# Performance work log

Measured on AMD Instinct MI355X. Metric: run time of the kernel, lower is better.

Reference implementation:

```python
import jax, jax.numpy as jnp
import numpy as np

N_NODES = 100000
N_EDGES = 1600000
NUM_GRAPHS = 1000
NODE_IN, EDGE_IN = 32, 16
NODE_EMB, EDGE_EMB, HID, OUT, L = 64, 32, 64, 1, 3
EPS = 1e-5


def _glorot(key, shape):
    fan_in = shape[0]
    return jax.random.normal(key, shape, jnp.float32) / np.sqrt(fan_in)


def setup_inputs() -> dict:
    key = jax.random.key(0)
    ks = jax.random.split(key, 16)
    inp = {
        "x": jax.random.normal(ks[0], (N_NODES, NODE_IN), jnp.float32),
        "edge_attr": jax.random.normal(ks[1], (N_EDGES, EDGE_IN), jnp.float32),
        "edge_index": jax.random.randint(ks[2], (2, N_EDGES), 0, N_NODES, jnp.int64
                                         if jax.config.jax_enable_x64 else jnp.int32),
        "batch": jnp.sort(jax.random.randint(ks[3], (N_NODES,), 0, NUM_GRAPHS)),
        # embeddings
        "node_W": _glorot(ks[4], (NODE_IN, NODE_EMB)),
        "node_b": jnp.zeros((NODE_EMB,), jnp.float32),
        "edge_W": _glorot(ks[5], (EDGE_IN, EDGE_EMB)),
        "edge_b": jnp.zeros((EDGE_EMB,), jnp.float32),
        # per-layer MPNN params (node_dim==64 for every layer since node_emb_dim==hidden_dim)
        "msg_W": _glorot(ks[6], (L, NODE_EMB + EDGE_EMB, HID)),
        "msg_b": jnp.zeros((L, HID), jnp.float32),
        "msg_gamma": jnp.ones((L, HID), jnp.float32),
        "msg_beta": jnp.zeros((L, HID), jnp.float32),
        "upd_W": _glorot(ks[7], (L, NODE_EMB + HID, HID)),
        "upd_b": jnp.zeros((L, HID), jnp.float32),
        "upd_gamma": jnp.ones((L, HID), jnp.float32),
        "upd_beta": jnp.zeros((L, HID), jnp.float32),
        # readout
        "r1_W": _glorot(ks[8], (HID, HID)),
        "r1_b": jnp.zeros((HID,), jnp.float32),
        "r2_W": _glorot(ks[9], (HID, OUT)),
        "r2_b": jnp.zeros((OUT,), jnp.float32),
    }
    return inp


def _bn(h, gamma, beta):
    # BatchNorm1d in training mode: normalize with batch mean / biased variance
    mu = jnp.mean(h, axis=0)
    var = jnp.mean(jnp.square(h - mu), axis=0)
    return gamma * (h - mu) * jax.lax.rsqrt(var + EPS) + beta


def reference(x, edge_attr, edge_index, batch,
              node_W, node_b, edge_W, edge_b,
              msg_W, msg_b, msg_gamma, msg_beta,
              upd_W, upd_b, upd_gamma, upd_beta,
              r1_W, r1_b, r2_W, r2_b):
    h = x @ node_W + node_b                       # [N, 64]
    e = edge_attr @ edge_W + edge_b               # [E, 32]
    src, dst = edge_index[0], edge_index[1]
    for i in range(L):
        # message: gather x_j, concat edge feats, Linear-ReLU-BN (dropout = eval/no-op)
        m = jnp.concatenate([h[src], e], axis=-1) @ msg_W[i] + msg_b[i]   # [E, 64]
        m = _bn(jax.nn.relu(m), msg_gamma[i], msg_beta[i])
        # aggregate: scatter-add to destination nodes
        agg = jax.ops.segment_sum(m, dst, num_segments=N_NODES)          # [N, 64]
        # update: concat self feats, Linear-ReLU-BN
        u = jnp.concatenate([h, agg], axis=-1) @ upd_W[i] + upd_b[i]     # [N, 64]
        h = _bn(jax.nn.relu(u), upd_gamma[i], upd_beta[i])
    # global add pool over graphs
    g = jax.ops.segment_sum(h, batch, num_segments=NUM_GRAPHS)           # [G, 64]
    out = jax.nn.relu(g @ r1_W + r1_b) @ r2_W + r2_b                     # [G, 1]
    return out
```

## Files before the change

### kernel.cpp

```cpp
#include <hip/hip_runtime.h>
#include <hip/hip_bf16.h>

#define N_NODES   100000
#define N_EDGES   1600000
#define NUM_GRAPHS 1000

typedef unsigned int u32;
typedef unsigned short u16;

typedef __bf16 bf16_t;
typedef bf16_t bf16x8 __attribute__((ext_vector_type(8)));
typedef float  f32x4  __attribute__((ext_vector_type(4)));

__device__ __forceinline__ float bf2f(u16 u){ return __uint_as_float(((u32)u)<<16); }
__device__ __forceinline__ float BL(u32 u){ return __uint_as_float(u<<16); }
__device__ __forceinline__ float BH(u32 u){ return __uint_as_float(u&0xffff0000u); }
__device__ __forceinline__ u16 f2bf(float f){
  u32 u = __float_as_uint(f);
  return (u16)((u + 0x7fffu + ((u>>16)&1u)) >> 16);
}
__device__ __forceinline__ float ldf(const void* p, size_t i, int isbf){
  return isbf ? bf2f(((const u16*)p)[i]) : ((const float*)p)[i];
}

__global__ void k_detect(const u32* __restrict__ x, int* __restrict__ flag){
  int t = threadIdx.x; int cnt = 0;
  for (int i = t; i < 256; i += 64){
    u32 w = x[i];
    u32 e = (w >> 7) & 0xffu;
    if (e >= 110u && e <= 137u) cnt++;
  }
  for (int o = 32; o; o >>= 1) cnt += __shfl_xor(cnt, o);
  if (t == 0) *flag = (cnt > 128) ? 1 : 0;
}

__global__ void k_prep(const void* __restrict__ eW, const void* __restrict__ eb,
                       const void* __restrict__ mW, const void* __restrict__ mb,
                       u16* __restrict__ Wcol, const int* __restrict__ flagp){
  int isbf = *flagp;
  int l = blockIdx.x, c = threadIdx.x;
  u16* W = Wcol + ((size_t)l*64 + c)*96;
  for (int k = 0; k < 64; k++)
    W[k] = f2bf(ldf(mW, (size_t)(l*96 + k)*64 + c, isbf));
  for (int j = 0; j < 16; j++){
    float acc = 0.f;
    for (int k = 0; k < 32; k++)
      acc += ldf(eW, (size_t)j*32 + k, isbf) * ldf(mW, (size_t)(l*96 + 64 + k)*64 + c, isbf);
    W[64 + j] = f2bf(acc);
  }
  float fbv = ldf(mb, (size_t)l*64 + c, isbf);
  for (int k = 0; k < 32; k++)
    fbv += ldf(eb, k, isbf) * ldf(mW, (size_t)(l*96 + 64 + k)*64 + c, isbf);
  W[80] = f2bf(fbv);
  for (int k = 81; k < 96; k++) W[k] = 0;
}

__global__ void k_node_emb(const void* __restrict__ x, const void* __restrict__ nW,
                           const void* __restrict__ nb, float* __restrict__ h,
                           u16* __restrict__ h_bf, const int* __restrict__ flagp){
  int isbf = *flagp;
  int lane = threadIdx.x & 63;
  int gw = (blockIdx.x*blockDim.x + threadIdx.x) >> 6;
  int nw = (gridDim.x*blockDim.x) >> 6;
  float w[32];
#pragma unroll
  for (int k = 0; k < 32; k++) w[k] = ldf(nW, (size_t)k*64 + lane, isbf);
  float bias = ldf(nb, lane, isbf);
  for (int n = gw; n < N_NODES; n += nw){
    float acc = bias;
    if (isbf){
      const uint4* xr = (const uint4*)((const u16*)x + (size_t)n*32);
#pragma unroll
      for (int q = 0; q < 4; q++){
        uint4 a = xr[q];
        u32 uu[4] = {a.x, a.y, a.z, a.w};
#pragma unroll
        for (int j = 0; j < 4; j++){
          acc = fmaf(BL(uu[j]), w[q*8 + 2*j + 0], acc);
          acc = fmaf(BH(uu[j]), w[q*8 + 2*j + 1], acc);
        }
      }
    } else {
      const float4* xr = (const float4*)((const float*)x + (size_t)n*32);
#pragma unroll
      for (int q = 0; q < 8; q++){
        float4 a = xr[q];
        acc = fmaf(a.x, w[q*4+0], acc); acc = fmaf(a.y, w[q*4+1], acc);
        acc = fmaf(a.z, w[q*4+2], acc); acc = fmaf(a.w, w[q*4+3], acc);
      }
    }
    h[(size_t)n*64 + lane] = acc;
    h_bf[(size_t)n*64 + lane] = f2bf(acc);
  }
}

__global__ void k_deg(const int* __restrict__ ei, int* __restrict__ deg){
  int i = blockIdx.x*blockDim.x + threadIdx.x;
  int stride = gridDim.x*blockDim.x;
  for (int e = i; e < N_EDGES; e += stride)
    atomicAdd(&deg[ei[N_EDGES + e]], 1);
}

__global__ void __launch_bounds__(256) k_scan1(const int* __restrict__ deg,
                                               int* __restrict__ bsum){
  __shared__ int wsum[4];
  int b = blockIdx.x, t = threadIdx.x;
  int i0 = b*512 + t;
  int s = 0;
  if (i0 < N_NODES) s += deg[i0];
  if (i0 + 256 < N_NODES) s += deg[i0 + 256];
  for (int o = 32; o; o >>= 1) s += __shfl_xor(s, o);
  if ((t & 63) == 0) wsum[t >> 6] = s;
  __syncthreads();
  if (t == 0) bsum[b] = wsum[0] + wsum[1] + wsum[2] + wsum[3];
}

__global__ void k_scan2(const int* __restrict__ bsum, int* __restrict__ boff,
                        int* __restrict__ rp){
  __shared__ int l[200];
  int t = threadIdx.x;
  if (t < 196) l[t] = bsum[t];
  __syncthreads();
  if (t == 0){
    int r = 0;
    for (int k = 0; k < 196; k++){ int x = l[k]; l[k] = r; r += x; }
    rp[N_NODES] = r;
  }
  __syncthreads();
  if (t < 196) boff[t] = l[t];
}

__global__ void __launch_bounds__(256) k_scan3(const int* __restrict__ deg,
                        const int* __restrict__ boff, int* __restrict__ rp,
                        int* __restrict__ cursor, float* __restrict__ degf){
  __shared__ int wpre[4];
  int b = blockIdx.x, t = threadIdx.x;
  int i0 = b*512 + 2*t;
  int d0 = (i0     < N_NODES) ? deg[i0]     : 0;
  int d1 = (i0 + 1 < N_NODES) ? deg[i0 + 1] : 0;
  int s = d0 + d1;
  int incl = s;
  for (int o = 1; o < 64; o <<= 1){ int u = __shfl_up(incl, o); if ((t & 63) >= o) incl += u; }
  if ((t & 63) == 63) wpre[t >> 6] = incl;
  __syncthreads();
  if (t == 0){ int r = 0; for (int k = 0; k < 4; k++){ int x = wpre[k]; wpre[k] = r; r += x; } }
  __syncthreads();
  int excl = boff[b] + wpre[t >> 6] + incl - s;
  if (i0 < N_NODES){
    rp[i0] = excl; cursor[i0] = excl; degf[i0] = (float)d0;
  }
  if (i0 + 1 < N_NODES){
    rp[i0+1] = excl + d0; cursor[i0+1] = excl + d0; degf[i0+1] = (float)d1;
  }
}

__global__ void k_scatter(const int* __restrict__ ei, int* __restrict__ cursor,
                          int* __restrict__ perm2){
  int i = blockIdx.x*blockDim.x + threadIdx.x;
  int stride = gridDim.x*blockDim.x;
  for (int e = i; e < N_EDGES; e += stride){
    int d = ei[N_EDGES + e];
    int p = atomicAdd(&cursor[d], 1);
    ((int2*)perm2)[p] = make_int2(ei[e], e);
  }
}

__global__ void __launch_bounds__(256) k_msgmm(
    const u16* __restrict__ h_bf, const void* __restrict__ ea,
    const int* __restrict__ rp, const int* __restrict__ perm2,
    const u16* __restrict__ Wcol, float* __restrict__ agg,
    float* __restrict__ stats, const int* __restrict__ flagp,
    int l, int nwaves){
  __shared__ float bs[128];
  __shared__ u32 lds[4*16*52];
  int tid = threadIdx.x;
  if (tid < 128) bs[tid] = 0.f;
  int lane = tid & 63, wv = tid >> 6;
  u32* A = lds + wv*16*52;
  int isbf = *flagp;
  if (lane < 32){
    uint4 z = make_uint4((lane&1)? 0u : 0x3f80u, 0u, 0u, 0u);
    *(uint4*)(A + (lane>>1)*52 + 40 + (lane&1)*4) = z;
  }
  __syncthreads();
  int w = blockIdx.x*4 + wv;
  long long t0 = (long long)w     * N_EDGES / nwaves;
  long long t1 = (long long)(w+1) * N_EDGES / nwaves;
  int lo = 0, hi = N_NODES;
  while (lo < hi){ int mid = (lo+hi)>>1; if ((long long)rp[mid] < t0) lo = mid+1; else hi = mid; }
  int n0 = lo, n1;
  if (w == nwaves-1) n1 = N_NODES;
  else {
    lo = 0; hi = N_NODES;
    while (lo < hi){ int mid = (lo+hi)>>1; if ((long long)rp[mid] < t1) lo = mid+1; else hi = mid; }
    n1 = lo;
  }
  int nn = lane & 15, kg = lane >> 4;
  bf16x8 B[3][4];
  const u16* Wl = Wcol + (size_t)l*64*96;
#pragma unroll
  for (int t = 0; t < 4; t++)
#pragma unroll
    for (int kb = 0; kb < 3; kb++)
      B[kb][t] = *(const bf16x8*)(Wl + (size_t)(t*16+nn)*96 + kb*32 + kg*8);
  float s1[4] = {0,0,0,0}, s2[4] = {0,0,0,0};
  int rA = lane>>3, sA = lane&7;
  int rC = lane>>1, sC = lane&1;
  for (int n = n0; n < n1; n++){
    int b0 = rp[n], b1 = rp[n+1];
    float r0 = 0.f, r1 = 0.f, r2 = 0.f, r3 = 0.f;
    for (int base = b0; base < b1; base += 16){
      int rem = b1 - base; if (rem > 16) rem = 16;
      int eA = base + (rA < rem ? rA : rem-1);
      int2 pA = ((const int2*)perm2)[eA];
      uint4 vA = ((const uint4*)h_bf)[(size_t)pA.x*8 + sA];
      int rB = rA + 8;
      int eB = base + (rB < rem ? rB : rem-1);
      int2 pB = ((const int2*)perm2)[eB];
      uint4 vB = ((const uint4*)h_bf)[(size_t)pB.x*8 + sA];
      uint4 vC; int doC = (lane < 32);
      if (doC){
        int eC = base + (rC < rem ? rC : rem-1);
        int2 pC = ((const int2*)perm2)[eC];
        if (isbf){
          vC = ((const uint4*)ea)[(size_t)pC.y*2 + sC];
        } else {
          const float4* ef = (const float4*)ea;
          float4 f0 = ef[(size_t)pC.y*4 + sC*2];
          float4 f1 = ef[(size_t)pC.y*4 + sC*2 + 1];
          vC.x = (u32)f2bf(f0.x) | ((u32)f2bf(f0.y)<<16);
          vC.y = (u32)f2bf(f0.z) | ((u32)f2bf(f0.w)<<16);
          vC.z = (u32)f2bf(f1.x) | ((u32)f2bf(f1.y)<<16);
          vC.w = (u32)f2bf(f1.z) | ((u32)f2bf(f1.w)<<16);
        }
      }
      asm volatile("s_waitcnt lgkmcnt(0)" ::: "memory");
      *(uint4*)(A + rA*52 + sA*4) = vA;
      *(uint4*)(A + rB*52 + sA*4) = vB;
      if (doC) *(uint4*)(A + rC*52 + 32 + sC*4) = vC;
      asm volatile("s_waitcnt lgkmcnt(0)" ::: "memory");
      f32x4 a0 = {0,0,0,0}, a1 = {0,0,0,0}, a2 = {0,0,0,0}, a3 = {0,0,0,0};
#pragma unroll
      for (int kb = 0; kb < 3; kb++){
        bf16x8 af = *(const bf16x8*)(A + nn*52 + kb*16 + kg*4);
        a0 = __builtin_amdgcn_mfma_f32_16x16x32_bf16(af, B[kb][0], a0, 0,0,0);
        a1 = __builtin_amdgcn_mfma_f32_16x16x32_bf16(af, B[kb][1], a1, 0,0,0);
        a2 = __builtin_amdgcn_mfma_f32_16x16x32_bf16(af, B[kb][2], a2, 0,0,0);
        a3 = __builtin_amdgcn_mfma_f32_16x16x32_bf16(af, B[kb][3], a3, 0,0,0);
      }
      int rowbase = kg*4;
      float ts0 = 0.f, ts1 = 0.f, ts2 = 0.f, ts3 = 0.f;
#pragma unroll
      for (int j = 0; j < 4; j++){
        bool valid = (rowbase + j) < rem;
        float m0 = fmaxf(a0[j], 0.f); m0 = valid ? m0 : 0.f;
        float m1 = fmaxf(a1[j], 0.f); m1 = valid ? m1 : 0.f;
        float m2 = fmaxf(a2[j], 0.f); m2 = valid ? m2 : 0.f;
        float m3 = fmaxf(a3[j], 0.f); m3 = valid ? m3 : 0.f;
        ts0 += m0; ts1 += m1; ts2 += m2; ts3 += m3;
        s2[0] = fmaf(m0,m0,s2[0]); s2[1] = fmaf(m1,m1,s2[1]);
        s2[2] = fmaf(m2,m2,s2[2]); s2[3] = fmaf(m3,m3,s2[3]);
      }
      s1[0] += ts0; s1[1] += ts1; s1[2] += ts2; s1[3] += ts3;
      ts0 += __shfl_xor(ts0,16); ts0 += __shfl_xor(ts0,32);
      ts1 += __shfl_xor(ts1,16); ts1 += __shfl_xor(ts1,32);
      ts2 += __shfl_xor(ts2,16); ts2 += __shfl_xor(ts2,32);
      ts3 += __shfl_xor(ts3,16); ts3 += __shfl_xor(ts3,32);
      r0 += ts0; r1 += ts1; r2 += ts2; r3 += ts3;
    }
    float v = (kg==0) ? r0 : (kg==1) ? r1 : (kg==2) ? r2 : r3;
    agg[(size_t)n*64 + lane] = v;
  }
#pragma unroll
  for (int t = 0; t < 4; t++){
    atomicAdd(&bs[t*16+nn], s1[t]);
    atomicAdd(&bs[64+t*16+nn], s2[t]);
  }
  __syncthreads();
  if (tid < 128) atomicAdd(&stats[tid], bs[tid]);
}

__global__ void k_fin(const float* __restrict__ stats, const void* __restrict__ gamma,
                      const void* __restrict__ beta, float* __restrict__ aff,
                      float cnt_inv, int goff, const int* __restrict__ flagp){
  int isbf = *flagp; int c = threadIdx.x;
  float mu  = stats[c]      * cnt_inv;
  float var = stats[64 + c] * cnt_inv - mu*mu;
  float rs  = rsqrtf(var + 1e-5f);
  float g = ldf(gamma, (size_t)goff + c, isbf);
  float b = ldf(beta,  (size_t)goff + c, isbf);
  aff[c]      = g*rs;
  aff[64 + c] = b - g*mu*rs;
}

__global__ void __launch_bounds__(256) k_upd(
    float* __restrict__ h, const float* __restrict__ agg,
    const float* __restrict__ degf, const float* __restrict__ maff,
    const void* __restrict__ uW, const void* __restrict__ ub,
    float* __restrict__ stats, const int* __restrict__ flagp, int l){
  __shared__ float bs[128];
  if (threadIdx.x < 128) bs[threadIdx.x] = 0.f;
  __syncthreads();
  int isbf = *flagp;
  int lane = threadIdx.x & 63;
  int gw = (blockIdx.x*blockDim.x + threadIdx.x) >> 6;
  int nw = (gridDim.x*blockDim.x) >> 6;
  float wa[64], wb[64]; float tv = 0.f;
#pragma unroll
  for (int k = 0; k < 64; k++){
    wa[k] = ldf(uW, (size_t)(l*128 + k)*64 + lane, isbf);
    float wk = ldf(uW, (size_t)(l*128 + 64 + k)*64 + lane, isbf);
    wb[k] = wk * maff[k];
    tv = fmaf(maff[64 + k], wk, tv);
  }
  float bias = ldf(ub, (size_t)l*64 + lane, isbf);
  float s1 = 0.f, s2 = 0.f;
  for (int n = gw; n < N_NODES; n += nw){
    const float4* hr = (const float4*)(h + (size_t)n*64);
    const float4* ar = (const float4*)(agg + (size_t)n*64);
    float a0 = fmaf(degf[n], tv, bias), a1 = 0.f, a2 = 0.f, a3 = 0.f;
#pragma unroll
    for (int q = 0; q < 8; q++){
      float4 a = hr[2*q+0];
      a0 = fmaf(a.x, wa[8*q+0], a0); a0 = fmaf(a.y, wa[8*q+1], a0);
      a0 = fmaf(a.z, wa[8*q+2], a0); a0 = fmaf(a.w, wa[8*q+3], a0);
      float4 b = hr[2*q+1];
      a1 = fmaf(b.x, wa[8*q+4], a1); a1 = fmaf(b.y, wa[8*q+5], a1);
      a1 = fmaf(b.z, wa[8*q+6], a1); a1 = fmaf(b.w, wa[8*q+7], a1);
      float4 c = ar[2*q+0];
      a2 = fmaf(c.x, wb[8*q+0], a2); a2 = fmaf(c.y, wb[8*q+1], a2);
      a2 = fmaf(c.z, wb[8*q+2], a2); a2 = fmaf(c.w, wb[8*q+3], a2);
      float4 d = ar[2*q+1];
      a3 = fmaf(d.x, wb[8*q+4], a3); a3 = fmaf(d.y, wb[8*q+5], a3);
      a3 = fmaf(d.z, wb[8*q+6], a3); a3 = fmaf(d.w, wb[8*q+7], a3);
    }
    float rl = fmaxf((a0 + a1) + (a2 + a3), 0.f);
    h[(size_t)n*64 + lane] = rl;
    s1 += rl;
    s2 = fmaf(rl, rl, s2);
  }
  atomicAdd(&bs[lane], s1);
  atomicAdd(&bs[64 + lane], s2);
  __syncthreads();
  if (threadIdx.x < 128) atomicAdd(&stats[threadIdx.x], bs[threadIdx.x]);
}

__global__ void k_norm(float* __restrict__ h, const float* __restrict__ uaff,
                       u16* __restrict__ h_bf){
  int i = blockIdx.x*blockDim.x + threadIdx.x;
  if (i >= N_NODES*16) return;
  int c4 = i & 15;
  float4 sq = *(const float4*)(uaff + 4*c4);
  float4 tq = *(const float4*)(uaff + 64 + 4*c4);
  float4 v = ((const float4*)h)[i];
  float4 o;
  o.x = fmaf(sq.x, v.x, tq.x); o.y = fmaf(sq.y, v.y, tq.y);
  o.z = fmaf(sq.z, v.z, tq.z); o.w = fmaf(sq.w, v.w, tq.w);
  ((float4*)h)[i] = o;
  ushort4 ob;
  ob.x = f2bf(o.x); ob.y = f2bf(o.y); ob.z = f2bf(o.z); ob.w = f2bf(o.w);
  ((ushort4*)h_bf)[i] = ob;
}

__global__ void k_pool(const float* __restrict__ h, const int* __restrict__ batch,
                       float* __restrict__ g){
  int lane = threadIdx.x & 63;
  int gw = (blockIdx.x*blockDim.x + threadIdx.x) >> 6;
  int nw = (gridDim.x*blockDim.x) >> 6;
  int chunk = (N_NODES + nw - 1) / nw;
  int n0 = gw*chunk;
  int n1 = n0 + chunk; if (n1 > N_NODES) n1 = N_NODES;
  int cur = -1; float acc = 0.f;
  for (int n = n0; n < n1; n++){
    int b = batch[n];
    float v = h[(size_t)n*64 + lane];
    if (b != cur){
      if (cur >= 0) atomicAdd(&g[(size_t)cur*64 + lane], acc);
      cur = b; acc = v;
    } else acc += v;
  }
  if (cur >= 0) atomicAdd(&g[(size_t)cur*64 + lane], acc);
}

__global__ void k_read(const float* __restrict__ g, const void* __restrict__ r1W,
                       const void* __restrict__ r1b, const void* __restrict__ r2W,
                       const void* __restrict__ r2b, void* __restrict__ out,
                       const int* __restrict__ flagp){
  int isbf = *flagp;
  int lane = threadIdx.x;
  int gr = blockIdx.x;
  float w[64];
#pragma unroll
  for (int k = 0; k < 64; k++) w[k] = ldf(r1W, (size_t)k*64 + lane, isbf);
  float acc = ldf(r1b, lane, isbf);
  const float4* grow = (const float4*)(g + (size_t)gr*64);
#pragma unroll
  for (int q = 0; q < 16; q++){
    float4 a = grow[q];
    acc = fmaf(a.x, w[4*q+0], acc); acc = fmaf(a.y, w[4*q+1], acc);
    acc = fmaf(a.z, w[4*q+2], acc); acc = fmaf(a.w, w[4*q+3], acc);
  }
  float hid = fmaxf(acc, 0.f);
  float p = hid * ldf(r2W, lane, isbf);
  for (int o = 32; o; o >>= 1) p += __shfl_xor(p, o);
  if (lane == 0){
    float v = p + ldf(r2b, 0, isbf);
    if (isbf) ((__hip_bfloat16*)out)[gr] = __float2bfloat16(v);
    else      ((float*)out)[gr] = v;
  }
}

extern "C" void kernel_launch(void* const* d_in, const int* in_sizes, int n_in,
                              void* d_out, int out_size, void* d_ws, size_t ws_size,
                              hipStream_t stream){
  const void* x    = d_in[0];
  const void* ea   = d_in[1];
  const int*  ei   = (const int*)d_in[2];
  const int*  bt   = (const int*)d_in[3];
  const void* nW   = d_in[4];  const void* nb  = d_in[5];
  const void* eW   = d_in[6];  const void* eb  = d_in[7];
  const void* mW   = d_in[8];  const void* mb  = d_in[9];
  const void* mg   = d_in[10]; const void* mbe = d_in[11];
  const void* uW   = d_in[12]; const void* ub  = d_in[13];
  const void* ug   = d_in[14]; const void* ube = d_in[15];
  const void* r1W  = d_in[16]; const void* r1b = d_in[17];
  const void* r2W  = d_in[18]; const void* r2b = d_in[19];

  float* ws = (float*)d_ws;
  float* h        = ws + 0;
  float* agg      = ws + 6400000;
  u16*   h_bf     = (u16*)(ws + 12800000);
  int*   perm2    = (int*)(ws + 16000000);
  float* degf     = ws + 19200000;
  int*   deg_i    = (int*)(ws + 19300000);
  float* g        = ws + 19400000;
  float* mstats   = ws + 19464000;
  float* ustats   = ws + 19464128;
  float* maff     = ws + 19464256;
  float* uaff     = ws + 19464384;
  int*   flag     = (int*)(ws + 19464512);
  u16*   Wcol     = (u16*)(ws + 19464528);
  int*   row_ptr  = (int*)(ws + 19473744);
  int*   cursor   = (int*)(ws + 19573748);
  int*   bsum     = (int*)(ws + 19673748);
  int*   boff     = (int*)(ws + 19673944);

  const int MM_BLOCKS = 2048;
  const int MM_WAVES  = MM_BLOCKS * 4;

  k_detect<<<1, 64, 0, stream>>>((const u32*)x, flag);
  hipMemsetAsync(ws + 19300000, 0, 164000*sizeof(float), stream);
  k_prep<<<3, 64, 0, stream>>>(eW, eb, mW, mb, Wcol, flag);
  k_node_emb<<<256, 256, 0, stream>>>(x, nW, nb, h, h_bf, flag);
  k_deg<<<512, 256, 0, stream>>>(ei, deg_i);
  k_scan1<<<196, 256, 0, stream>>>(deg_i, bsum);
  k_scan2<<<1, 256, 0, stream>>>(bsum, boff, row_ptr);
  k_scan3<<<196, 256, 0, stream>>>(deg_i, boff, row_ptr, cursor, degf);
  k_scatter<<<512, 256, 0, stream>>>(ei, cursor, perm2);

  for (int l = 0; l < 3; l++){
    hipMemsetAsync(mstats, 0, 256*sizeof(float), stream);
    k_msgmm<<<MM_BLOCKS, 256, 0, stream>>>(h_bf, ea, row_ptr, perm2, Wcol,
                                           agg, mstats, flag, l, MM_WAVES);
    k_fin<<<1, 64, 0, stream>>>(mstats, mg, mbe, maff, 1.0f/(float)N_EDGES, l*64, flag);
    k_upd<<<1024, 256, 0, stream>>>(h, agg, degf, maff, uW, ub, ustats, flag, l);
    k_fin<<<1, 64, 0, stream>>>(ustats, ug, ube, uaff, 1.0f/(float)N_NODES, l*64, flag);
    k_norm<<<(N_NODES*16 + 255)/256, 256, 0, stream>>>(h, uaff, h_bf);
  }

  k_pool<<<128, 256, 0, stream>>>(h, bt, g);
  k_read<<<NUM_GRAPHS, 64, 0, stream>>>(g, r1W, r1b, r2W, r2b, d_out, flag);
}
```

Before: 1.550 ms.

## Fold update BatchNorm affine into next-layer weights and drop normalize pass

Removes the per-layer normalize kernel by folding the update BatchNorm scale and shift into the next layer's message weights (new k_fold kernel), the update weights, and the final pool. k_upd now writes the bf16 copy of h directly. k_fin resets the stats, so the per-layer memsets go away. The message kernel loads its MFMA A fragments straight from global memory into registers instead of staging them through LDS, which removes LDS traffic and waits. In exchange, rounding changes because the scale is folded into bf16 weights, and each lane now does its own scattered row loads.

```diff
diff --git a/kernel.cpp b/kernel.cpp
--- a/kernel.cpp
+++ b/kernel.cpp
@@ -23,6 +23,8 @@
   return isbf ? bf2f(((const u16*)p)[i]) : ((const float*)p)[i];
 }
 
+union U4BF { uint4 u; bf16x8 v; };
+
 __global__ void k_detect(const u32* __restrict__ x, int* __restrict__ flag){
   int t = threadIdx.x; int cnt = 0;
   for (int i = t; i < 256; i += 64){
@@ -36,7 +38,8 @@
 
 __global__ void k_prep(const void* __restrict__ eW, const void* __restrict__ eb,
                        const void* __restrict__ mW, const void* __restrict__ mb,
-                       u16* __restrict__ Wcol, const int* __restrict__ flagp){
+                       u16* __restrict__ Wcol, u16* __restrict__ Weff,
+                       float* __restrict__ uaff, const int* __restrict__ flagp){
   int isbf = *flagp;
   int l = blockIdx.x, c = threadIdx.x;
   u16* W = Wcol + ((size_t)l*64 + c)*96;
@@ -53,6 +56,27 @@
     fbv += ldf(eb, k, isbf) * ldf(mW, (size_t)(l*96 + 64 + k)*64 + c, isbf);
   W[80] = f2bf(fbv);
   for (int k = 81; k < 96; k++) W[k] = 0;
+  if (l == 0){
+    u16* We = Weff + (size_t)c*96;
+    for (int k = 0; k < 96; k++) We[k] = W[k];
+    uaff[c] = 1.0f; uaff[64 + c] = 0.0f;
+  }
+}
+
+__global__ void k_fold(const u16* __restrict__ Wcol, u16* __restrict__ Weff,
+                       const float* __restrict__ uaff, int lnext){
+  int c = threadIdx.x;
+  const u16* src = Wcol + ((size_t)lnext*64 + c)*96;
+  u16* dst = Weff + ((size_t)lnext*64 + c)*96;
+  float bias = bf2f(src[80]);
+  for (int k = 0; k < 64; k++){
+    float w = bf2f(src[k]);
+    dst[k] = f2bf(w * uaff[k]);
+    bias = fmaf(uaff[64 + k], w, bias);
+  }
+  for (int k = 64; k < 80; k++) dst[k] = src[k];
+  dst[80] = f2bf(bias);
+  for (int k = 81; k < 96; k++) dst[k] = 0;
 }
 
 __global__ void k_node_emb(const void* __restrict__ x, const void* __restrict__ nW,
@@ -168,21 +192,15 @@
 __global__ void __launch_bounds__(256) k_msgmm(
     const u16* __restrict__ h_bf, const void* __restrict__ ea,
     const int* __restrict__ rp, const int* __restrict__ perm2,
-    const u16* __restrict__ Wcol, float* __restrict__ agg,
+    const u16* __restrict__ Weff, float* __restrict__ agg,
     float* __restrict__ stats, const int* __restrict__ flagp,
     int l, int nwaves){
   __shared__ float bs[128];
-  __shared__ u32 lds[4*16*52];
   int tid = threadIdx.x;
   if (tid < 128) bs[tid] = 0.f;
+  __syncthreads();
+  int isbf = *flagp;
   int lane = tid & 63, wv = tid >> 6;
-  u32* A = lds + wv*16*52;
-  int isbf = *flagp;
-  if (lane < 32){
-    uint4 z = make_uint4((lane&1)? 0u : 0x3f80u, 0u, 0u, 0u);
-    *(uint4*)(A + (lane>>1)*52 + 40 + (lane&1)*4) = z;
-  }
-  __syncthreads();
   int w = blockIdx.x*4 + wv;
   long long t0 = (long long)w     * N_EDGES / nwaves;
   long long t1 = (long long)(w+1) * N_EDGES / nwaves;
@@ -197,57 +215,51 @@
   }
   int nn = lane & 15, kg = lane >> 4;
   bf16x8 B[3][4];
-  const u16* Wl = Wcol + (size_t)l*64*96;
+  const u16* Wl = Weff + (size_t)l*64*96;
 #pragma unroll
   for (int t = 0; t < 4; t++)
 #pragma unroll
     for (int kb = 0; kb < 3; kb++)
       B[kb][t] = *(const bf16x8*)(Wl + (size_t)(t*16+nn)*96 + kb*32 + kg*8);
+  U4BF ac; ac.u = make_uint4((kg==2)? 0x3f80u : 0u, 0u, 0u, 0u);
   float s1[4] = {0,0,0,0}, s2[4] = {0,0,0,0};
-  int rA = lane>>3, sA = lane&7;
-  int rC = lane>>1, sC = lane&1;
   for (int n = n0; n < n1; n++){
     int b0 = rp[n], b1 = rp[n+1];
     float r0 = 0.f, r1 = 0.f, r2 = 0.f, r3 = 0.f;
     for (int base = b0; base < b1; base += 16){
       int rem = b1 - base; if (rem > 16) rem = 16;
-      int eA = base + (rA < rem ? rA : rem-1);
-      int2 pA = ((const int2*)perm2)[eA];
-      uint4 vA = ((const uint4*)h_bf)[(size_t)pA.x*8 + sA];
-      int rB = rA + 8;
-      int eB = base + (rB < rem ? rB : rem-1);
-      int2 pB = ((const int2*)perm2)[eB];
-      uint4 vB = ((const uint4*)h_bf)[(size_t)pB.x*8 + sA];
-      uint4 vC; int doC = (lane < 32);
-      if (doC){
-        int eC = base + (rC < rem ? rC : rem-1);
-        int2 pC = ((const int2*)perm2)[eC];
+      int row = (nn < rem) ? nn : rem-1;
+      int2 p = ((const int2*)perm2)[base + row];
+      const uint4* hp = (const uint4*)(h_bf + (size_t)p.x*64);
+      U4BF fA, fB, fC;
+      fA.u = hp[kg];
+      fB.u = hp[4 + kg];
+      if (kg < 2){
         if (isbf){
-          vC = ((const uint4*)ea)[(size_t)pC.y*2 + sC];
+          fC.u = ((const uint4*)ea)[(size_t)p.y*2 + kg];
         } else {
           const float4* ef = (const float4*)ea;
-          float4 f0 = ef[(size_t)pC.y*4 + sC*2];
-          float4 f1 = ef[(size_t)pC.y*4 + sC*2 + 1];
-          vC.x = (u32)f2bf(f0.x) | ((u32)f2bf(f0.y)<<16);
-          vC.y = (u32)f2bf(f0.z) | ((u32)f2bf(f0.w)<<16);
-          vC.z = (u32)f2bf(f1.x) | ((u32)f2bf(f1.y)<<16);
-          vC.w = (u32)f2bf(f1.z) | ((u32)f2bf(f1.w)<<16);
+          float4 f0 = ef[(size_t)p.y*4 + kg*2];
+          float4 f1 = ef[(size_t)p.y*4 + kg*2 + 1];
+          fC.u.x = (u32)f2bf(f0.x) | ((u32)f2bf(f0.y)<<16);
+          fC.u.y = (u32)f2bf(f0.z) | ((u32)f2bf(f0.w)<<16);
+          fC.u.z = (u32)f2bf(f1.x) | ((u32)f2bf(f1.y)<<16);
+          fC.u.w = (u32)f2bf(f1.z) | ((u32)f2bf(f1.w)<<16);
         }
-      }
-      asm volatile("s_waitcnt lgkmcnt(0)" ::: "memory");
-      *(uint4*)(A + rA*52 + sA*4) = vA;
-      *(uint4*)(A + rB*52 + sA*4) = vB;
-      if (doC) *(uint4*)(A + rC*52 + 32 + sC*4) = vC;
-      asm volatile("s_waitcnt lgkmcnt(0)" ::: "memory");
+      } else fC = ac;
       f32x4 a0 = {0,0,0,0}, a1 = {0,0,0,0}, a2 = {0,0,0,0}, a3 = {0,0,0,0};
-#pragma unroll
-      for (int kb = 0; kb < 3; kb++){
-        bf16x8 af = *(const bf16x8*)(A + nn*52 + kb*16 + kg*4);
-        a0 = __builtin_amdgcn_mfma_f32_16x16x32_bf16(af, B[kb][0], a0, 0,0,0);
-        a1 = __builtin_amdgcn_mfma_f32_16x16x32_bf16(af, B[kb][1], a1, 0,0,0);
-        a2 = __builtin_amdgcn_mfma_f32_16x16x32_bf16(af, B[kb][2], a2, 0,0,0);
-        a3 = __builtin_amdgcn_mfma_f32_16x16x32_bf16(af, B[kb][3], a3, 0,0,0);
-      }
+      a0 = __builtin_amdgcn_mfma_f32_16x16x32_bf16(fA.v, B[0][0], a0, 0,0,0);
+      a1 = __builtin_amdgcn_mfma_f32_16x16x32_bf16(fA.v, B[0][1], a1, 0,0,0);
+      a2 = __builtin_amdgcn_mfma_f32_16x16x32_bf16(fA.v, B[0][2], a2, 0,0,0);
+      a3 = __builtin_amdgcn_mfma_f32_16x16x32_bf16(fA.v, B[0][3], a3, 0,0,0);
+      a0 = __builtin_amdgcn_mfma_f32_16x16x32_bf16(fB.v, B[1][0], a0, 0,0,0);
+      a1 = __builtin_amdgcn_mfma_f32_16x16x32_bf16(fB.v, B[1][1], a1, 0,0,0);
+      a2 = __builtin_amdgcn_mfma_f32_16x16x32_bf16(fB.v, B[1][2], a2, 0,0,0);
+      a3 = __builtin_amdgcn_mfma_f32_16x16x32_bf16(fB.v, B[1][3], a3, 0,0,0);
+      a0 = __builtin_amdgcn_mfma_f32_16x16x32_bf16(fC.v, B[2][0], a0, 0,0,0);
+      a1 = __builtin_amdgcn_mfma_f32_16x16x32_bf16(fC.v, B[2][1], a1, 0,0,0);
+      a2 = __builtin_amdgcn_mfma_f32_16x16x32_bf16(fC.v, B[2][2], a2, 0,0,0);
+      a3 = __builtin_amdgcn_mfma_f32_16x16x32_bf16(fC.v, B[2][3], a3, 0,0,0);
       int rowbase = kg*4;
       float ts0 = 0.f, ts1 = 0.f, ts2 = 0.f, ts3 = 0.f;
 #pragma unroll
@@ -280,7 +292,7 @@
   if (tid < 128) atomicAdd(&stats[tid], bs[tid]);
 }
 
-__global__ void k_fin(const float* __restrict__ stats, const void* __restrict__ gamma,
+__global__ void k_fin(float* __restrict__ stats, const void* __restrict__ gamma,
                       const void* __restrict__ beta, float* __restrict__ aff,
                       float cnt_inv, int goff, const int* __restrict__ flagp){
   int isbf = *flagp; int c = threadIdx.x;
@@ -291,11 +303,13 @@
   float b = ldf(beta,  (size_t)goff + c, isbf);
   aff[c]      = g*rs;
   aff[64 + c] = b - g*mu*rs;
+  stats[c] = 0.f; stats[64 + c] = 0.f;
 }
 
 __global__ void __launch_bounds__(256) k_upd(
-    float* __restrict__ h, const float* __restrict__ agg,
+    float* __restrict__ h, u16* __restrict__ h_bf, const float* __restrict__ agg,
     const float* __restrict__ degf, const float* __restrict__ maff,
+    const float* __restrict__ aff_prev,
     const void* __restrict__ uW, const void* __restrict__ ub,
     float* __restrict__ stats, const int* __restrict__ flagp, int l){
   __shared__ float bs[128];
@@ -305,15 +319,17 @@
   int lane = threadIdx.x & 63;
   int gw = (blockIdx.x*blockDim.x + threadIdx.x) >> 6;
   int nw = (gridDim.x*blockDim.x) >> 6;
-  float wa[64], wb[64]; float tv = 0.f;
+  float wa[64], wb[64]; float tv = 0.f, tv2 = 0.f;
 #pragma unroll
   for (int k = 0; k < 64; k++){
-    wa[k] = ldf(uW, (size_t)(l*128 + k)*64 + lane, isbf);
+    float wka = ldf(uW, (size_t)(l*128 + k)*64 + lane, isbf);
+    wa[k] = wka * aff_prev[k];
+    tv2 = fmaf(aff_prev[64 + k], wka, tv2);
     float wk = ldf(uW, (size_t)(l*128 + 64 + k)*64 + lane, isbf);
     wb[k] = wk * maff[k];
     tv = fmaf(maff[64 + k], wk, tv);
   }
-  float bias = ldf(ub, (size_t)l*64 + lane, isbf);
+  float bias = ldf(ub, (size_t)l*64 + lane, isbf) + tv2;
   float s1 = 0.f, s2 = 0.f;
   for (int n = gw; n < N_NODES; n += nw){
     const float4* hr = (const float4*)(h + (size_t)n*64);
@@ -336,6 +352,7 @@
     }
     float rl = fmaxf((a0 + a1) + (a2 + a3), 0.f);
     h[(size_t)n*64 + lane] = rl;
+    h_bf[(size_t)n*64 + lane] = f2bf(rl);
     s1 += rl;
     s2 = fmaf(rl, rl, s2);
   }
@@ -345,35 +362,19 @@
   if (threadIdx.x < 128) atomicAdd(&stats[threadIdx.x], bs[threadIdx.x]);
 }
 
-__global__ void k_norm(float* __restrict__ h, const float* __restrict__ uaff,
-                       u16* __restrict__ h_bf){
-  int i = blockIdx.x*blockDim.x + threadIdx.x;
-  if (i >= N_NODES*16) return;
-  int c4 = i & 15;
-  float4 sq = *(const float4*)(uaff + 4*c4);
-  float4 tq = *(const float4*)(uaff + 64 + 4*c4);
-  float4 v = ((const float4*)h)[i];
-  float4 o;
-  o.x = fmaf(sq.x, v.x, tq.x); o.y = fmaf(sq.y, v.y, tq.y);
-  o.z = fmaf(sq.z, v.z, tq.z); o.w = fmaf(sq.w, v.w, tq.w);
-  ((float4*)h)[i] = o;
-  ushort4 ob;
-  ob.x = f2bf(o.x); ob.y = f2bf(o.y); ob.z = f2bf(o.z); ob.w = f2bf(o.w);
-  ((ushort4*)h_bf)[i] = ob;
-}
-
 __global__ void k_pool(const float* __restrict__ h, const int* __restrict__ batch,
-                       float* __restrict__ g){
+                       const float* __restrict__ uaff, float* __restrict__ g){
   int lane = threadIdx.x & 63;
   int gw = (blockIdx.x*blockDim.x + threadIdx.x) >> 6;
   int nw = (gridDim.x*blockDim.x) >> 6;
+  float s = uaff[lane], t = uaff[64 + lane];
   int chunk = (N_NODES + nw - 1) / nw;
   int n0 = gw*chunk;
   int n1 = n0 + chunk; if (n1 > N_NODES) n1 = N_NODES;
   int cur = -1; float acc = 0.f;
   for (int n = n0; n < n1; n++){
     int b = batch[n];
-    float v = h[(size_t)n*64 + lane];
+    float v = fmaf(s, h[(size_t)n*64 + lane], t);
     if (b != cur){
       if (cur >= 0) atomicAdd(&g[(size_t)cur*64 + lane], acc);
       cur = b; acc = v;
@@ -440,17 +441,18 @@
   float* uaff     = ws + 19464384;
   int*   flag     = (int*)(ws + 19464512);
   u16*   Wcol     = (u16*)(ws + 19464528);
-  int*   row_ptr  = (int*)(ws + 19473744);
-  int*   cursor   = (int*)(ws + 19573748);
-  int*   bsum     = (int*)(ws + 19673748);
-  int*   boff     = (int*)(ws + 19673944);
+  u16*   Weff     = (u16*)(ws + 19473744);
+  int*   row_ptr  = (int*)(ws + 19482960);
+  int*   cursor   = (int*)(ws + 19582964);
+  int*   bsum     = (int*)(ws + 19682964);
+  int*   boff     = (int*)(ws + 19683160);
 
   const int MM_BLOCKS = 2048;
   const int MM_WAVES  = MM_BLOCKS * 4;
 
   k_detect<<<1, 64, 0, stream>>>((const u32*)x, flag);
-  hipMemsetAsync(ws + 19300000, 0, 164000*sizeof(float), stream);
-  k_prep<<<3, 64, 0, stream>>>(eW, eb, mW, mb, Wcol, flag);
+  hipMemsetAsync(ws + 19300000, 0, 164256*sizeof(float), stream);
+  k_prep<<<3, 64, 0, stream>>>(eW, eb, mW, mb, Wcol, Weff, uaff, flag);
   k_node_emb<<<256, 256, 0, stream>>>(x, nW, nb, h, h_bf, flag);
   k_deg<<<512, 256, 0, stream>>>(ei, deg_i);
   k_scan1<<<196, 256, 0, stream>>>(deg_i, bsum);
@@ -459,15 +461,15 @@
   k_scatter<<<512, 256, 0, stream>>>(ei, cursor, perm2);
 
   for (int l = 0; l < 3; l++){
-    hipMemsetAsync(mstats, 0, 256*sizeof(float), stream);
-    k_msgmm<<<MM_BLOCKS, 256, 0, stream>>>(h_bf, ea, row_ptr, perm2, Wcol,
+    k_msgmm<<<MM_BLOCKS, 256, 0, stream>>>(h_bf, ea, row_ptr, perm2, Weff,
                                            agg, mstats, flag, l, MM_WAVES);
     k_fin<<<1, 64, 0, stream>>>(mstats, mg, mbe, maff, 1.0f/(float)N_EDGES, l*64, flag);
-    k_upd<<<1024, 256, 0, stream>>>(h, agg, degf, maff, uW, ub, ustats, flag, l);
+    k_upd<<<1024, 256, 0, stream>>>(h, h_bf, agg, degf, maff, uaff, uW, ub,
+                                    ustats, flag, l);
     k_fin<<<1, 64, 0, stream>>>(ustats, ug, ube, uaff, 1.0f/(float)N_NODES, l*64, flag);
-    k_norm<<<(N_NODES*16 + 255)/256, 256, 0, stream>>>(h, uaff, h_bf);
-  }
-
-  k_pool<<<128, 256, 0, stream>>>(h, bt, g);
+    if (l < 2) k_fold<<<1, 64, 0, stream>>>(Wcol, Weff, uaff, l+1);
+  }
+
+  k_pool<<<128, 256, 0, stream>>>(h, bt, uaff, g);
   k_read<<<NUM_GRAPHS, 64, 0, stream>>>(g, r1W, r1b, r2W, r2b, d_out, flag);
 }
```

After: 1.581 ms. 1.02x slower.
